# Performance work log

Measured on AMD Instinct MI355X. Metric: run time of the kernel, lower is better.

## Reference

```python
import jax, jax.numpy as jnp
import numpy as np

B, C, H, W = 8, 1152, 32, 32
N = H * W


def _skew(t):
    # t: (B,3) -> (B,3,3) skew-symmetric
    z = jnp.zeros_like(t[:, 0])
    return jnp.stack([
        jnp.stack([z, -t[:, 2], t[:, 1]], axis=-1),
        jnp.stack([t[:, 2], z, -t[:, 0]], axis=-1),
        jnp.stack([-t[:, 1], t[:, 0], z], axis=-1),
    ], axis=1)


def _fundamental(K1, K2, R, t):
    E = _skew(t) @ R
    U, S, Vt = jnp.linalg.svd(E)
    S = S.at[:, 2].set(0.0)  # enforce rank-2 essential matrix
    E = U @ (S[:, :, None] * Vt)
    return jnp.linalg.inv(jnp.swapaxes(K2, 1, 2)) @ E @ jnp.linalg.inv(K1)


def setup_inputs() -> dict:
    key = jax.random.key(0)
    k1, k2, k3, k4, k5 = jax.random.split(key, 5)
    f_tar = jax.random.normal(k1, (B, C, H, W), dtype=jnp.float32)
    f_src = jax.random.normal(k2, (B, C, H, W), dtype=jnp.float32)
    # realistic invertible intrinsics: [[fx,0,cx],[0,fy,cy],[0,0,1]]
    def intrinsics(k):
        f = 30.0 + 2.0 * jax.random.uniform(k, (B, 2))
        Kt = jnp.zeros((B, 3, 3))
        Kt = Kt.at[:, 0, 0].set(f[:, 0]).at[:, 1, 1].set(f[:, 1])
        Kt = Kt.at[:, 0, 2].set(W / 2.0).at[:, 1, 2].set(H / 2.0).at[:, 2, 2].set(1.0)
        return Kt.astype(jnp.float32)
    K1 = intrinsics(k3)
    K2 = intrinsics(k4)
    # proper rotation via QR of a random matrix
    ka, kb = jax.random.split(k5)
    Q, Rm = jnp.linalg.qr(jax.random.normal(ka, (B, 3, 3)))
    Q = Q * jnp.sign(jnp.diagonal(Rm, axis1=1, axis2=2))[:, None, :]
    Q = Q * jnp.linalg.det(Q)[:, None, None]  # det = +1
    t = jax.random.normal(kb, (B, 3), dtype=jnp.float32)
    return {"f_tar": f_tar, "f_src": f_src, "K1": K1, "K2": K2,
            "R": Q.astype(jnp.float32), "t": t}


def reference(f_tar, f_src, K1, K2, R, t):
    f_src_flat = f_src.reshape(B, C, N)  # (B,C,N)
    # NOTE: torch code computes A = f_src^T @ f_tar but never uses it (dead code); omitted.

    # homogeneous pixel coords, indexing='ij': x=row index, y=col index
    ix, iy = jnp.meshgrid(jnp.arange(H, dtype=jnp.float32),
                          jnp.arange(W, dtype=jnp.float32), indexing='ij')
    combined = jnp.stack([ix.ravel(), iy.ravel(), jnp.ones(N, jnp.float32)], axis=0)  # (3,N)
    combined = jnp.broadcast_to(combined, (B, 3, N))

    F_mat = _fundamental(K1, K2, R, t)                       # (B,3,3)
    lines = F_mat @ combined                                 # (B,3,N)
    lines = lines / lines[:, 2:3, :]

    ones = jnp.ones((B, 1, N), jnp.float32)
    x0 = jnp.zeros((B, 1, N), jnp.float32)
    y0 = -lines[:, 2:3, :] / lines[:, 1:2, :]
    point_0 = jnp.concatenate([x0, y0, ones], axis=1)        # (B,3,N)
    x1 = jnp.full((B, 1, N), float(W), jnp.float32)
    y1 = -(lines[:, 2:3, :] + lines[:, 0:1, :] * W) / lines[:, 1:2, :]
    point_1 = jnp.concatenate([x1, y1, ones], axis=1)        # (B,3,N)

    # point-to-line distance for every (pixel i, line j) pair -> (B,N,N)
    diff = point_0 - point_1                                 # (B,3,N)
    p = combined[:, :, :, None] - point_0[:, :, None, :]     # (B,3,N,N) via broadcast
    d = diff[:, :, None, :]                                  # (B,3,1,N)
    cross = jnp.stack([
        p[:, 1] * d[:, 2] - p[:, 2] * d[:, 1],
        p[:, 2] * d[:, 0] - p[:, 0] * d[:, 2],
        p[:, 0] * d[:, 1] - p[:, 1] * d[:, 0],
    ], axis=1)                                               # (B,3,N,N)
    cross_norm = jnp.sqrt(jnp.sum(cross * cross, axis=1))    # (B,N,N)
    diff_norm = jnp.linalg.norm(diff, axis=1, keepdims=True) # (B,1,N)
    d_epi = cross_norm / diff_norm                           # (B,N,N)

    thre = 0.1
    weight_map = 1.0 - jax.nn.softmax(5.0 * (d_epi - thre), axis=-1)
    attention_map = jax.nn.softmax(weight_map, axis=1)       # softmax over dim=1, per torch code

    out = jnp.einsum('bij,bjc->bic', attention_map, jnp.swapaxes(f_src_flat, 1, 2))  # (B,N,C)
    return out.reshape(B, C, H, W)
```

## Files before the change

kernel.cpp:

```cpp
#include <hip/hip_runtime.h>
#include <hip/hip_bf16.h>
#include <math.h>

#define Bn 8
#define Cn 1152
#define Hn 32
#define Wn 32
#define Nn 1024

typedef short short8 __attribute__((ext_vector_type(8)));
typedef float f32x4 __attribute__((ext_vector_type(4)));

__device__ float g_rmax[Bn * Nn];
__device__ float g_rsuminv[Bn * Nn];
__device__ float g_csum_part[Bn * 8 * Nn];
__device__ unsigned short g_A[(size_t)Bn * Nn * Nn];
__device__ unsigned short g_fb[(size_t)Bn * Cn * Nn];

__device__ inline unsigned short f2bf(float x) {
    __hip_bfloat16 h = __float2bfloat16(x);
    unsigned short u;
    __builtin_memcpy(&u, &h, 2);
    return u;
}

__device__ inline void inv3(const float* M, float* o) {
    float a = M[0], b = M[1], c = M[2];
    float d = M[3], e = M[4], f = M[5];
    float g = M[6], h = M[7], i = M[8];
    float A0 = (e * i - f * h);
    float A1 = -(d * i - f * g);
    float A2 = (d * h - e * g);
    float det = a * A0 + b * A1 + c * A2;
    float inv = 1.0f / det;
    o[0] = A0 * inv;
    o[1] = -(b * i - c * h) * inv;
    o[2] = (b * f - c * e) * inv;
    o[3] = A1 * inv;
    o[4] = (a * i - c * g) * inv;
    o[5] = -(a * f - c * d) * inv;
    o[6] = A2 * inv;
    o[7] = -(a * h - b * g) * inv;
    o[8] = (a * e - b * d) * inv;
}

__device__ inline void mm3(const float* X, const float* Y, float* Z) {
    for (int r = 0; r < 3; r++)
        for (int c = 0; c < 3; c++)
            Z[r * 3 + c] = X[r * 3 + 0] * Y[0 * 3 + c] + X[r * 3 + 1] * Y[1 * 3 + c] +
                           X[r * 3 + 2] * Y[2 * 3 + c];
}

__device__ inline void computeF(const float* K1, const float* K2, const float* R,
                                const float* t, int b, float* F) {
    float t0 = t[b * 3 + 0], t1 = t[b * 3 + 1], t2 = t[b * 3 + 2];
    float S[9] = {0.0f, -t2, t1, t2, 0.0f, -t0, -t1, t0, 0.0f};
    float E[9];
    mm3(S, &R[b * 9], E);
    float iK1[9], iK2[9];
    inv3(&K1[b * 9], iK1);
    inv3(&K2[b * 9], iK2);
    float iK2T[9] = {iK2[0], iK2[3], iK2[6], iK2[1], iK2[4], iK2[7], iK2[2], iK2[5], iK2[8]};
    float T[9];
    mm3(iK2T, E, T);
    mm3(T, iK1, F);
}

__device__ inline void lineparams(const float* F, int j, float& dy, float& y0, float& invn) {
    float ix = (float)(j >> 5);
    float iy = (float)(j & 31);
    float l0 = F[0] * ix + F[1] * iy + F[2];
    float l1 = F[3] * ix + F[4] * iy + F[5];
    float l2 = F[6] * ix + F[7] * iy + F[8];
    l0 = l0 / l2;
    l1 = l1 / l2;
    y0 = -1.0f / l1;
    float y1 = -(1.0f + l0 * 32.0f) / l1;
    dy = y0 - y1;
    invn = 1.0f / sqrtf(1024.0f + dy * dy);
}

__device__ inline float zval(float ix, float iy, float dy, float y0, float invn) {
    float d = fabsf(ix * dy + 32.0f * (iy - y0)) * invn;
    return 5.0f * (d - 0.1f);
}

__global__ void rowstats_kernel(const float* __restrict__ K1, const float* __restrict__ K2,
                                const float* __restrict__ R, const float* __restrict__ t) {
    int lin = blockIdx.x;
    int b = lin & 7;
    int seg = lin >> 3;
    float F[9];
    computeF(K1, K2, R, t, b, F);
    int wv = threadIdx.x >> 6;
    int lane = threadIdx.x & 63;
    int i = seg * 4 + wv;
    float ix = (float)(i >> 5), iy = (float)(i & 31);
    float z[16];
    float m = -INFINITY;
#pragma unroll
    for (int k = 0; k < 16; k++) {
        int j = lane + k * 64;
        float dy, y0, invn;
        lineparams(F, j, dy, y0, invn);
        z[k] = zval(ix, iy, dy, y0, invn);
        m = fmaxf(m, z[k]);
    }
#pragma unroll
    for (int o = 32; o > 0; o >>= 1) m = fmaxf(m, __shfl_xor(m, o, 64));
    float s = 0.0f;
#pragma unroll
    for (int k = 0; k < 16; k++) s += __expf(z[k] - m);
#pragma unroll
    for (int o = 32; o > 0; o >>= 1) s += __shfl_xor(s, o, 64);
    if (lane == 0) {
        g_rmax[b * Nn + i] = m;
        g_rsuminv[b * Nn + i] = 1.0f / s;
    }
}

__global__ void colE_kernel(const float* __restrict__ K1, const float* __restrict__ K2,
                            const float* __restrict__ R, const float* __restrict__ t) {
    int lin = blockIdx.x;
    int b = lin & 7;
    int r = lin >> 3;
    int jt = r & 15;
    int it = r >> 4;
    float F[9];
    computeF(K1, K2, R, t, b, F);
    int tt = threadIdx.x;
    int jloc = tt & 63;
    int ig = tt >> 6;
    int j = jt * 64 + jloc;
    int base = b * Nn;
    float dy, y0, invn;
    lineparams(F, j, dy, y0, invn);
    float csump = 0.0f;
#pragma unroll 4
    for (int k = 0; k < 32; k++) {
        int i = it * 128 + ig * 32 + k;
        float rmax = g_rmax[base + i];
        float rsi = g_rsuminv[base + i];
        float ix = (float)(i >> 5), iy = (float)(i & 31);
        float z = zval(ix, iy, dy, y0, invn);
        float s1 = __expf(z - rmax) * rsi;
        float E = __expf(1.0f - s1);
        csump += E;
        g_A[((size_t)base + i) * Nn + j] = f2bf(E);
    }
    __shared__ float red[4][64];
    red[ig][jloc] = csump;
    __syncthreads();
    if (ig == 0) {
        float s = red[0][jloc] + red[1][jloc] + red[2][jloc] + red[3][jloc];
        g_csum_part[(b * 8 + it) * Nn + j] = s;
    }
}

__global__ void convert_fsrc_kernel(const float* __restrict__ f) {
    int lin = blockIdx.x;
    int b = lin & 7;
    int c = lin >> 3;
    int j = threadIdx.x * 4;
    float4 cs = *(const float4*)&g_csum_part[(b * 8 + 0) * Nn + j];
#pragma unroll
    for (int it = 1; it < 8; it++) {
        float4 p = *(const float4*)&g_csum_part[(b * 8 + it) * Nn + j];
        cs.x += p.x; cs.y += p.y; cs.z += p.z; cs.w += p.w;
    }
    size_t off = ((size_t)b * Cn + c) * Nn + j;
    float4 v = *(const float4*)(f + off);
    ushort4 u;
    u.x = f2bf(v.x / cs.x);
    u.y = f2bf(v.y / cs.y);
    u.z = f2bf(v.z / cs.z);
    u.w = f2bf(v.w / cs.w);
    *(ushort4*)&g_fb[off] = u;
}

#define BM 128
#define BNc 128
#define BK 32

__launch_bounds__(256) __global__ void gemm_kernel(float* __restrict__ out) {
    __shared__ unsigned short As[2][BM * BK];
    __shared__ unsigned short Bs[2][BNc * BK];
    int lin = blockIdx.x;
    int b = lin & 7;
    int s = lin >> 3;
    int it = s / 9;
    int ct = s - it * 9;
    int i0 = it * BM;
    int c0 = ct * BNc;
    int t = threadIdx.x;
    int w = t >> 6, L = t & 63;
    int wm = w >> 1, wn = w & 1;
    const unsigned short* Ab = g_A + (size_t)b * Nn * Nn + (size_t)i0 * Nn;
    const unsigned short* Fb = g_fb + (size_t)b * Cn * Nn + (size_t)c0 * Nn;

    auto stage = [&](int p, int kt) {
#pragma unroll
        for (int h = 0; h < 2; h++) {
            int chunk = (h * 4 + w) * 64 + L;
            int rr = chunk >> 2;
            int gq = (chunk & 3) ^ ((rr >> 1) & 3);
            const unsigned short* ga = Ab + (size_t)rr * Nn + kt + gq * 8;
            const unsigned short* gb = Fb + (size_t)rr * Nn + kt + gq * 8;
            __builtin_amdgcn_global_load_lds(
                (const __attribute__((address_space(1))) unsigned int*)ga,
                (__attribute__((address_space(3))) unsigned int*)(As[p] + chunk * 8), 16, 0, 0);
            __builtin_amdgcn_global_load_lds(
                (const __attribute__((address_space(1))) unsigned int*)gb,
                (__attribute__((address_space(3))) unsigned int*)(Bs[p] + chunk * 8), 16, 0, 0);
        }
    };

    f32x4 acc[4][4] = {};
    int lrow = L & 15, quad = L >> 4;
    stage(0, 0);
    for (int kt = 0; kt < Nn; kt += BK) {
        int p = (kt >> 5) & 1;
        __syncthreads();
        if (kt + BK < Nn) stage(1 - p, kt + BK);
        short8 af[4], bf[4];
#pragma unroll
        for (int mt = 0; mt < 4; mt++) {
            int rr = wm * 64 + mt * 16 + lrow;
            int q = quad ^ ((rr >> 1) & 3);
            af[mt] = *(const short8*)(As[p] + rr * BK + q * 8);
        }
#pragma unroll
        for (int nt = 0; nt < 4; nt++) {
            int rr = wn * 64 + nt * 16 + lrow;
            int q = quad ^ ((rr >> 1) & 3);
            bf[nt] = *(const short8*)(Bs[p] + rr * BK + q * 8);
        }
#pragma unroll
        for (int mt = 0; mt < 4; mt++)
#pragma unroll
            for (int nt = 0; nt < 4; nt++)
                acc[mt][nt] =
                    __builtin_amdgcn_mfma_f32_16x16x32_bf16(af[mt], bf[nt], acc[mt][nt], 0, 0, 0);
    }
#pragma unroll
    for (int mt = 0; mt < 4; mt++)
#pragma unroll
        for (int rg = 0; rg < 4; rg++) {
            int i = i0 + wm * 64 + mt * 16 + quad * 4 + rg;
            float* orow = out + ((size_t)b * Nn + i) * Cn + c0 + wn * 64;
#pragma unroll
            for (int nt = 0; nt < 4; nt++) orow[nt * 16 + quad * 0 + (L & 15)] = acc[mt][nt][rg];
        }
}

extern "C" void kernel_launch(void* const* d_in, const int* in_sizes, int n_in,
                              void* d_out, int out_size, void* d_ws, size_t ws_size,
                              hipStream_t stream) {
    (void)in_sizes; (void)n_in; (void)d_ws; (void)ws_size; (void)out_size;
    const float* f_src = (const float*)d_in[1];
    const float* K1 = (const float*)d_in[2];
    const float* K2 = (const float*)d_in[3];
    const float* R = (const float*)d_in[4];
    const float* t = (const float*)d_in[5];
    float* out = (float*)d_out;

    rowstats_kernel<<<dim3(2048), dim3(256), 0, stream>>>(K1, K2, R, t);
    colE_kernel<<<dim3(1024), dim3(256), 0, stream>>>(K1, K2, R, t);
    convert_fsrc_kernel<<<dim3(Bn * Cn), dim3(256), 0, stream>>>(f_src);
    gemm_kernel<<<dim3(Bn * (Nn / BM) * (Cn / BNc)), dim3(256), 0, stream>>>(out);
}
```

Measured before the change: 198.8 us.

## Precompute line coefficients, vectorize colE stores, batch fsrc conversion, retile GEMM

Per-line epipolar coefficients are folded into three scalars so each distance becomes two FMAs and an abs. rowstats caches them in shared memory, and colE computes four columns per thread with vectorized bf16 stores and a shared-memory column reduction. The f_src conversion handles eight channels per block using reciprocal multiplies instead of divides. The GEMM moves to 128x64 tiles with 128 threads, which gives more blocks but less data reuse per block.

```diff
diff --git a/kernel.cpp b/kernel.cpp
--- a/kernel.cpp
+++ b/kernel.cpp
@@ -66,32 +66,36 @@
     mm3(T, iK1, F);
 }
 
-__device__ inline void lineparams(const float* F, int j, float& dy, float& y0, float& invn) {
-    float ix = (float)(j >> 5);
-    float iy = (float)(j & 31);
-    float l0 = F[0] * ix + F[1] * iy + F[2];
-    float l1 = F[3] * ix + F[4] * iy + F[5];
-    float l2 = F[6] * ix + F[7] * iy + F[8];
+__device__ inline float4 zcoef(const float* F, int j) {
+    float jx = (float)(j >> 5);
+    float jy = (float)(j & 31);
+    float l0 = F[0] * jx + F[1] * jy + F[2];
+    float l1 = F[3] * jx + F[4] * jy + F[5];
+    float l2 = F[6] * jx + F[7] * jy + F[8];
     l0 = l0 / l2;
     l1 = l1 / l2;
-    y0 = -1.0f / l1;
+    float y0 = -1.0f / l1;
     float y1 = -(1.0f + l0 * 32.0f) / l1;
-    dy = y0 - y1;
-    invn = 1.0f / sqrtf(1024.0f + dy * dy);
-}
-
-__device__ inline float zval(float ix, float iy, float dy, float y0, float invn) {
-    float d = fabsf(ix * dy + 32.0f * (iy - y0)) * invn;
-    return 5.0f * (d - 0.1f);
+    float dy = y0 - y1;
+    float invn = 1.0f / sqrtf(1024.0f + dy * dy);
+    return make_float4(5.0f * dy * invn, 160.0f * invn, 160.0f * y0 * invn, 0.0f);
 }
 
 __global__ void rowstats_kernel(const float* __restrict__ K1, const float* __restrict__ K2,
                                 const float* __restrict__ R, const float* __restrict__ t) {
+    __shared__ float Fs[9];
+    __shared__ float4 prm[Nn];
     int lin = blockIdx.x;
     int b = lin & 7;
     int seg = lin >> 3;
-    float F[9];
-    computeF(K1, K2, R, t, b, F);
+    if (threadIdx.x == 0) computeF(K1, K2, R, t, b, Fs);
+    __syncthreads();
+#pragma unroll
+    for (int u = 0; u < 4; u++) {
+        int j = threadIdx.x * 4 + u;
+        prm[j] = zcoef(Fs, j);
+    }
+    __syncthreads();
     int wv = threadIdx.x >> 6;
     int lane = threadIdx.x & 63;
     int i = seg * 4 + wv;
@@ -100,10 +104,8 @@
     float m = -INFINITY;
 #pragma unroll
     for (int k = 0; k < 16; k++) {
-        int j = lane + k * 64;
-        float dy, y0, invn;
-        lineparams(F, j, dy, y0, invn);
-        z[k] = zval(ix, iy, dy, y0, invn);
+        float4 p = prm[lane + k * 64];
+        z[k] = fabsf(fmaf(ix, p.x, fmaf(iy, p.y, -p.z))) - 0.5f;
         m = fmaxf(m, z[k]);
     }
 #pragma unroll
@@ -121,94 +123,121 @@
 
 __global__ void colE_kernel(const float* __restrict__ K1, const float* __restrict__ K2,
                             const float* __restrict__ R, const float* __restrict__ t) {
+    __shared__ float Fs[9];
+    __shared__ float rm[128], rs[128];
+    __shared__ float4 red[16][16];
     int lin = blockIdx.x;
     int b = lin & 7;
     int r = lin >> 3;
     int jt = r & 15;
     int it = r >> 4;
-    float F[9];
-    computeF(K1, K2, R, t, b, F);
     int tt = threadIdx.x;
-    int jloc = tt & 63;
-    int ig = tt >> 6;
-    int j = jt * 64 + jloc;
-    int base = b * Nn;
-    float dy, y0, invn;
-    lineparams(F, j, dy, y0, invn);
-    float csump = 0.0f;
-#pragma unroll 4
-    for (int k = 0; k < 32; k++) {
-        int i = it * 128 + ig * 32 + k;
-        float rmax = g_rmax[base + i];
-        float rsi = g_rsuminv[base + i];
+    if (tt < 128) {
+        rm[tt] = g_rmax[b * Nn + it * 128 + tt];
+        rs[tt] = g_rsuminv[b * Nn + it * 128 + tt];
+    }
+    if (tt == 0) computeF(K1, K2, R, t, b, Fs);
+    __syncthreads();
+    int tcol = tt & 15, trow = tt >> 4;
+    int j0 = jt * 64 + tcol * 4;
+    float4 p0 = zcoef(Fs, j0 + 0);
+    float4 p1 = zcoef(Fs, j0 + 1);
+    float4 p2 = zcoef(Fs, j0 + 2);
+    float4 p3 = zcoef(Fs, j0 + 3);
+    float4 csum = make_float4(0.f, 0.f, 0.f, 0.f);
+#pragma unroll
+    for (int k = 0; k < 8; k++) {
+        int il = trow + k * 16;
+        float rmax = rm[il], rsi = rs[il];
+        int i = it * 128 + il;
         float ix = (float)(i >> 5), iy = (float)(i & 31);
-        float z = zval(ix, iy, dy, y0, invn);
-        float s1 = __expf(z - rmax) * rsi;
-        float E = __expf(1.0f - s1);
-        csump += E;
-        g_A[((size_t)base + i) * Nn + j] = f2bf(E);
-    }
-    __shared__ float red[4][64];
-    red[ig][jloc] = csump;
+        float z0 = fabsf(fmaf(ix, p0.x, fmaf(iy, p0.y, -p0.z))) - 0.5f;
+        float z1 = fabsf(fmaf(ix, p1.x, fmaf(iy, p1.y, -p1.z))) - 0.5f;
+        float z2 = fabsf(fmaf(ix, p2.x, fmaf(iy, p2.y, -p2.z))) - 0.5f;
+        float z3 = fabsf(fmaf(ix, p3.x, fmaf(iy, p3.y, -p3.z))) - 0.5f;
+        float E0 = __expf(1.0f - __expf(z0 - rmax) * rsi);
+        float E1 = __expf(1.0f - __expf(z1 - rmax) * rsi);
+        float E2 = __expf(1.0f - __expf(z2 - rmax) * rsi);
+        float E3 = __expf(1.0f - __expf(z3 - rmax) * rsi);
+        csum.x += E0; csum.y += E1; csum.z += E2; csum.w += E3;
+        ushort4 u;
+        u.x = f2bf(E0); u.y = f2bf(E1); u.z = f2bf(E2); u.w = f2bf(E3);
+        *(ushort4*)&g_A[((size_t)b * Nn + i) * Nn + j0] = u;
+    }
+    red[trow][tcol] = csum;
     __syncthreads();
-    if (ig == 0) {
-        float s = red[0][jloc] + red[1][jloc] + red[2][jloc] + red[3][jloc];
-        g_csum_part[(b * 8 + it) * Nn + j] = s;
+    if (tt < 16) {
+        float4 s = red[0][tt];
+#pragma unroll
+        for (int q = 1; q < 16; q++) {
+            float4 p = red[q][tt];
+            s.x += p.x; s.y += p.y; s.z += p.z; s.w += p.w;
+        }
+        *(float4*)&g_csum_part[(b * 8 + it) * Nn + jt * 64 + tt * 4] = s;
     }
 }
 
 __global__ void convert_fsrc_kernel(const float* __restrict__ f) {
     int lin = blockIdx.x;
     int b = lin & 7;
-    int c = lin >> 3;
-    int j = threadIdx.x * 4;
-    float4 cs = *(const float4*)&g_csum_part[(b * 8 + 0) * Nn + j];
+    int cg = lin >> 3;
+    int j0 = threadIdx.x * 4;
+    float4 cs = *(const float4*)&g_csum_part[(b * 8 + 0) * Nn + j0];
 #pragma unroll
     for (int it = 1; it < 8; it++) {
-        float4 p = *(const float4*)&g_csum_part[(b * 8 + it) * Nn + j];
+        float4 p = *(const float4*)&g_csum_part[(b * 8 + it) * Nn + j0];
         cs.x += p.x; cs.y += p.y; cs.z += p.z; cs.w += p.w;
     }
-    size_t off = ((size_t)b * Cn + c) * Nn + j;
-    float4 v = *(const float4*)(f + off);
-    ushort4 u;
-    u.x = f2bf(v.x / cs.x);
-    u.y = f2bf(v.y / cs.y);
-    u.z = f2bf(v.z / cs.z);
-    u.w = f2bf(v.w / cs.w);
-    *(ushort4*)&g_fb[off] = u;
+    float4 inv = make_float4(1.0f / cs.x, 1.0f / cs.y, 1.0f / cs.z, 1.0f / cs.w);
+#pragma unroll
+    for (int c8 = 0; c8 < 8; c8++) {
+        int c = cg * 8 + c8;
+        size_t off = ((size_t)b * Cn + c) * Nn + j0;
+        float4 v = *(const float4*)(f + off);
+        ushort4 u;
+        u.x = f2bf(v.x * inv.x);
+        u.y = f2bf(v.y * inv.y);
+        u.z = f2bf(v.z * inv.z);
+        u.w = f2bf(v.w * inv.w);
+        *(ushort4*)&g_fb[off] = u;
+    }
 }
 
 #define BM 128
-#define BNc 128
+#define BNc 64
 #define BK 32
 
-__launch_bounds__(256) __global__ void gemm_kernel(float* __restrict__ out) {
+__launch_bounds__(128) __global__ void gemm_kernel(float* __restrict__ out) {
     __shared__ unsigned short As[2][BM * BK];
     __shared__ unsigned short Bs[2][BNc * BK];
     int lin = blockIdx.x;
     int b = lin & 7;
     int s = lin >> 3;
-    int it = s / 9;
-    int ct = s - it * 9;
+    int it = s & 7;
+    int ct = s >> 3;
     int i0 = it * BM;
     int c0 = ct * BNc;
     int t = threadIdx.x;
     int w = t >> 6, L = t & 63;
-    int wm = w >> 1, wn = w & 1;
     const unsigned short* Ab = g_A + (size_t)b * Nn * Nn + (size_t)i0 * Nn;
     const unsigned short* Fb = g_fb + (size_t)b * Cn * Nn + (size_t)c0 * Nn;
 
     auto stage = [&](int p, int kt) {
 #pragma unroll
         for (int h = 0; h < 2; h++) {
-            int chunk = (h * 4 + w) * 64 + L;
+            int chunk = h * 128 + t;
             int rr = chunk >> 2;
             int gq = (chunk & 3) ^ ((rr >> 1) & 3);
             const unsigned short* ga = Ab + (size_t)rr * Nn + kt + gq * 8;
-            const unsigned short* gb = Fb + (size_t)rr * Nn + kt + gq * 8;
             __builtin_amdgcn_global_load_lds(
                 (const __attribute__((address_space(1))) unsigned int*)ga,
                 (__attribute__((address_space(3))) unsigned int*)(As[p] + chunk * 8), 16, 0, 0);
+        }
+        {
+            int chunk = t;
+            int rr = chunk >> 2;
+            int gq = (chunk & 3) ^ ((rr >> 1) & 3);
+            const unsigned short* gb = Fb + (size_t)rr * Nn + kt + gq * 8;
             __builtin_amdgcn_global_load_lds(
                 (const __attribute__((address_space(1))) unsigned int*)gb,
                 (__attribute__((address_space(3))) unsigned int*)(Bs[p] + chunk * 8), 16, 0, 0);
@@ -217,23 +246,47 @@
 
     f32x4 acc[4][4] = {};
     int lrow = L & 15, quad = L >> 4;
-    stage(0, 0);
+    auto stage2 = [&](int p, int kt) {
+#pragma unroll
+        for (int h = 0; h < 4; h++) {
+            int chunk = h * 128 + t;
+            int rr = chunk >> 2;
+            int gq = (chunk & 3) ^ ((rr >> 1) & 3);
+            const unsigned short* ga = Ab + (size_t)rr * Nn + kt + gq * 8;
+            __builtin_amdgcn_global_load_lds(
+                (const __attribute__((address_space(1))) unsigned int*)ga,
+                (__attribute__((address_space(3))) unsigned int*)(As[p] + chunk * 8), 16, 0, 0);
+        }
+#pragma unroll
+        for (int h = 0; h < 2; h++) {
+            int chunk = h * 128 + t;
+            int rr = chunk >> 2;
+            int gq = (chunk & 3) ^ ((rr >> 1) & 3);
+            const unsigned short* gb = Fb + (size_t)rr * Nn + kt + gq * 8;
+            __builtin_amdgcn_global_load_lds(
+                (const __attribute__((address_space(1))) unsigned int*)gb,
+                (__attribute__((address_space(3))) unsigned int*)(Bs[p] + chunk * 8), 16, 0, 0);
+        }
+    };
+    (void)stage;
+
+    stage2(0, 0);
     for (int kt = 0; kt < Nn; kt += BK) {
         int p = (kt >> 5) & 1;
         __syncthreads();
-        if (kt + BK < Nn) stage(1 - p, kt + BK);
+        if (kt + BK < Nn) stage2(1 - p, kt + BK);
         short8 af[4], bf[4];
 #pragma unroll
         for (int mt = 0; mt < 4; mt++) {
-            int rr = wm * 64 + mt * 16 + lrow;
+            int rr = w * 64 + mt * 16 + lrow;
             int q = quad ^ ((rr >> 1) & 3);
             af[mt] = *(const short8*)(As[p] + rr * BK + q * 8);
         }
 #pragma unroll
         for (int nt = 0; nt < 4; nt++) {
-            int rr = wn * 64 + nt * 16 + lrow;
-            int q = quad ^ ((rr >> 1) & 3);
-            bf[nt] = *(const short8*)(Bs[p] + rr * BK + q * 8);
+            int cc = nt * 16 + lrow;
+            int q = quad ^ ((cc >> 1) & 3);
+            bf[nt] = *(const short8*)(Bs[p] + cc * BK + q * 8);
         }
 #pragma unroll
         for (int mt = 0; mt < 4; mt++)
@@ -242,14 +295,15 @@
                 acc[mt][nt] =
                     __builtin_amdgcn_mfma_f32_16x16x32_bf16(af[mt], bf[nt], acc[mt][nt], 0, 0, 0);
     }
+    int col = L & 15;
 #pragma unroll
     for (int mt = 0; mt < 4; mt++)
 #pragma unroll
         for (int rg = 0; rg < 4; rg++) {
-            int i = i0 + wm * 64 + mt * 16 + quad * 4 + rg;
-            float* orow = out + ((size_t)b * Nn + i) * Cn + c0 + wn * 64;
-#pragma unroll
-            for (int nt = 0; nt < 4; nt++) orow[nt * 16 + quad * 0 + (L & 15)] = acc[mt][nt][rg];
+            int i = i0 + w * 64 + mt * 16 + quad * 4 + rg;
+            float* orow = out + ((size_t)b * Nn + i) * Cn + c0;
+#pragma unroll
+            for (int nt = 0; nt < 4; nt++) orow[nt * 16 + col] = acc[mt][nt][rg];
         }
 }
 
@@ -266,6 +320,6 @@
 
     rowstats_kernel<<<dim3(2048), dim3(256), 0, stream>>>(K1, K2, R, t);
     colE_kernel<<<dim3(1024), dim3(256), 0, stream>>>(K1, K2, R, t);
-    convert_fsrc_kernel<<<dim3(Bn * Cn), dim3(256), 0, stream>>>(f_src);
-    gemm_kernel<<<dim3(Bn * (Nn / BM) * (Cn / BNc)), dim3(256), 0, stream>>>(out);
-}
+    convert_fsrc_kernel<<<dim3(Bn * Cn / 8), dim3(256), 0, stream>>>(f_src);
+    gemm_kernel<<<dim3(Bn * (Nn / BM) * (Cn / BNc)), dim3(128), 0, stream>>>(out);
+}
```

Measured after the change: 171.4 us. 13.8% less time.
